# Performance work log

Hardware: AMD Instinct MI355X
Metric: run time of the kernel (lower is better)

The kernel has to match this reference:

```python
import jax, jax.numpy as jnp
import numpy as np

KNOTS = 8
INTERVAL = 4.0
LAYERS = 8
WIDTH = 128
DX = 64
DY = 64
P = 3 * KNOTS - 1  # widths(K) + heights(K) + interior derivatives(K-1)
BATCH = 16384
MIN_DERIV = 1e-3
SOFTMAX_ADJ = 1e-2


def _made_masks(D, W):
    in_deg = np.arange(1, D + 1)
    hid_deg = (np.arange(W) % max(D - 1, 1)) + 1
    m1 = (hid_deg[:, None] >= in_deg[None, :]).astype(np.float32)        # (W, D)
    out_deg = np.repeat(np.arange(1, D + 1), P)                           # (D*P,)
    m2 = (out_deg[:, None] > hid_deg[None, :]).astype(np.float32)        # (D*P, W)
    return jnp.asarray(m1), jnp.asarray(m2)


def _adj_softmax(v):
    p = jax.nn.softmax(v, axis=-1)
    return (p + SOFTMAX_ADJ / v.shape[-1]) / (1.0 + SOFTMAX_ADJ)


def _rqs_transform(x, params):
    # x: (B, D); params: (B, D, P). Rational-quadratic spline on [-B_int, B_int], identity outside.
    Bi = INTERVAL
    w = params[..., :KNOTS]
    h = params[..., KNOTS:2 * KNOTS]
    d = params[..., 2 * KNOTS:]
    widths = _adj_softmax(w) * 2 * Bi
    heights = _adj_softmax(h) * 2 * Bi
    zero = jnp.zeros(x.shape + (1,), x.dtype)
    x_pos = -Bi + jnp.concatenate([zero, jnp.cumsum(widths, -1)], -1)   # (B, D, K+1)
    y_pos = -Bi + jnp.concatenate([zero, jnp.cumsum(heights, -1)], -1)
    derivs = jax.nn.softplus(d) + MIN_DERIV                              # (B, D, K-1)
    one = jnp.ones(x.shape + (1,), x.dtype)
    derivs = jnp.concatenate([one, derivs, one], -1)                     # (B, D, K+1), boundary derivs = 1
    inside = (x > -Bi) & (x < Bi)
    xc = jnp.clip(x, -Bi, Bi)
    # bin search (K is small; vectorized comparison)
    k = jnp.clip(jnp.sum((xc[..., None] >= x_pos), -1) - 1, 0, KNOTS - 1)

    def g(a, i):
        return jnp.take_along_axis(a, i[..., None], -1)[..., 0]

    xk, xk1 = g(x_pos, k), g(x_pos, k + 1)
    yk, yk1 = g(y_pos, k), g(y_pos, k + 1)
    dk, dk1 = g(derivs, k), g(derivs, k + 1)
    sk = (yk1 - yk) / (xk1 - xk)
    xi = (xc - xk) / (xk1 - xk)
    omx = 1.0 - xi
    den = sk + (dk1 + dk - 2.0 * sk) * xi * omx
    out = yk + (yk1 - yk) * (sk * xi * xi + dk * xi * omx) / den
    ld = 2.0 * jnp.log(sk) + jnp.log(dk1 * xi * xi + 2.0 * sk * xi * omx + dk * omx * omx) - 2.0 * jnp.log(den)
    return jnp.where(inside, out, x), jnp.where(inside, ld, 0.0)


def _maf_transform(x, W1, b1, Wout, bout, D):
    # Stacked layers: masked MLP -> elementwise RQ spline -> reverse permutation.
    m1, m2 = _made_masks(D, WIDTH)

    def layer(carry, ws):
        xc, ld = carry
        w1, bb1, wo, bo = ws
        hdn = jax.nn.relu(xc @ (w1 * m1).T + bb1)                # (B, W)
        p = (hdn @ (wo * m2).T + bo).reshape(xc.shape[0], D, P)  # (B, D, P)
        x2, ldj = _rqs_transform(xc, p)
        return (x2[:, ::-1], ld + ldj.sum(-1)), None

    init = (x, jnp.zeros(x.shape[0], x.dtype))
    (xf, ld), _ = jax.lax.scan(layer, init, (W1, b1, Wout, bout))
    return xf, ld


def setup_inputs() -> dict:
    key = jax.random.key(0)
    ks = jax.random.split(key, 10)
    s = 0.05
    return {
        "x": jax.random.normal(ks[0], (BATCH, DX), jnp.float32),
        "y": jax.random.normal(ks[1], (BATCH, DY), jnp.float32),
        "f_W1": jax.random.normal(ks[2], (LAYERS, WIDTH, DX), jnp.float32) * s,
        "f_b1": jnp.zeros((LAYERS, WIDTH), jnp.float32),
        "f_Wout": jax.random.normal(ks[3], (LAYERS, DX * P, WIDTH), jnp.float32) * s,
        "f_bout": jnp.zeros((LAYERS, DX * P), jnp.float32),
        "g_W1": jax.random.normal(ks[4], (LAYERS, WIDTH, DY), jnp.float32) * s,
        "g_b1": jnp.zeros((LAYERS, WIDTH), jnp.float32),
        "g_Wout": jax.random.normal(ks[5], (LAYERS, DY * P, WIDTH), jnp.float32) * s,
        "g_bout": jnp.zeros((LAYERS, DY * P), jnp.float32),
    }


def reference(x, y, f_W1, f_b1, f_Wout, f_bout, g_W1, g_b1, g_Wout, g_bout):
    xo, ldf = _maf_transform(x, f_W1, f_b1, f_Wout, f_bout, DX)
    yo, ldg = _maf_transform(y, g_W1, g_b1, g_Wout, g_bout, DY)
    return (xo, ldf, yo, ldg)
```

## Files before the change

kernel.cpp:

```cpp
#include <hip/hip_runtime.h>
#include <math.h>

#define BATCH   16384
#define DIMS    64
#define WID     128
#define KN      8
#define NP      23
#define NCOL    (DIMS * NP)
#define NLAYERS 8
#define BI_F    4.0f
#define GRP     92
#define NGRP    16
#define XPITCH  68
#define LOG2E   1.44269504f

#define PF_WOUT (NLAYERS * NCOL * WID)
#define PF_W1   (NLAYERS * WID * DIMS)

typedef short s16x8 __attribute__((ext_vector_type(8)));
typedef float f32x4 __attribute__((ext_vector_type(4)));

__device__ __forceinline__ unsigned short f2bf(float f) {
    unsigned int u = __builtin_bit_cast(unsigned int, f);
    unsigned int r = (u + 0x7FFFu + ((u >> 16) & 1u)) >> 16;
    return (unsigned short)r;
}
__device__ __forceinline__ float bf2f(unsigned short u) {
    return __builtin_bit_cast(float, (unsigned int)u << 16);
}
__device__ __forceinline__ unsigned int cvtpk_bf16(float a, float b) {
    unsigned int r;
    asm("v_cvt_pk_bf16_f32 %0, %1, %2" : "=v"(r) : "v"(a), "v"(b));
    return r;
}

__device__ __forceinline__ void stage16(const unsigned short* g, unsigned short* l) {
    __builtin_amdgcn_global_load_lds(
        (__attribute__((address_space(1))) void*)g,
        (__attribute__((address_space(3))) void*)l,
        16, 0, 0);
}

__global__ __launch_bounds__(256) void premask_kernel(
    const float* __restrict__ f_wout, const float* __restrict__ g_wout,
    const float* __restrict__ f_w1,   const float* __restrict__ g_w1,
    unsigned short* __restrict__ womask, unsigned short* __restrict__ w1mask)
{
    const int idx    = blockIdx.x * 256 + threadIdx.x;
    const int stride = gridDim.x * 256;

    const int totw = 2 * PF_WOUT;
    for (int i = idx; i < totw; i += stride) {
        int fl = i / PF_WOUT;
        int r  = i % PF_WOUT;
        int h  = r % WID;
        int o  = (r / WID) % NCOL;
        int d  = o / NP;
        int hd = h % (DIMS - 1) + 1;
        const float* src = fl ? g_wout : f_wout;
        unsigned short v = (hd <= d) ? f2bf(src[r] * LOG2E) : (unsigned short)0;
        const int dst = i - h + (h ^ ((o & 7) << 4));
        womask[dst] = v;
    }

    const int tot1 = 2 * PF_W1;
    for (int i = idx; i < tot1; i += stride) {
        int fl = i / PF_W1;
        int r  = i % PF_W1;
        int c  = r % DIMS;
        int w  = (r / DIMS) % WID;
        int deg = w % (DIMS - 1) + 1;
        const float* src = fl ? g_w1 : f_w1;
        w1mask[i] = (c < deg) ? f2bf(src[r]) : (unsigned short)0;
    }
}

__global__ __launch_bounds__(256)
__attribute__((amdgpu_waves_per_eu(2, 2)))
void flow8_kernel(
    const float* __restrict__ xin_f, const float* __restrict__ xin_g,
    float* __restrict__ xout_f,      float* __restrict__ xout_g,
    const unsigned short* __restrict__ w1m_f, const unsigned short* __restrict__ w1m_g,
    const float* __restrict__ b1_f,  const float* __restrict__ b1_g,
    const unsigned short* __restrict__ wom_f, const unsigned short* __restrict__ wom_g,
    const float* __restrict__ bo_f,  const float* __restrict__ bo_g,
    float* __restrict__ ld_f,        float* __restrict__ ld_g)
{
    __shared__ __align__(16) unsigned short Wl[GRP * WID];
    __shared__ __align__(16) unsigned short S[4][2176];
    __shared__ __align__(16) float Xf[2][4][16][XPITCH];

    const int t    = threadIdx.x;
    const int wv   = t >> 6;
    const int ln   = t & 63;
    const int m    = ln & 15;
    const int q    = ln >> 4;
    const int flow = blockIdx.y;
    const int r0   = blockIdx.x * 64 + wv * 16;

    const float* xin          = flow ? xin_g : xin_f;
    float*       xout         = flow ? xout_g : xout_f;
    const unsigned short* w1m = flow ? w1m_g : w1m_f;
    const float* b1           = flow ? b1_g  : b1_f;
    const unsigned short* wom = flow ? wom_g : wom_f;
    const float* bo           = flow ? bo_g  : bo_f;
    float*       ldp          = flow ? ld_g  : ld_f;

    {
        const int row = ln >> 2;
        const int c0  = (ln & 3) * 16;
        const float* srcr = xin + (size_t)(r0 + row) * DIMS + c0;
        float* dstr = &Xf[0][wv][row][c0];
        #pragma unroll
        for (int i = 0; i < 4; ++i)
            *(float4*)(dstr + i * 4) = *(const float4*)(srcr + i * 4);
    }
    asm volatile("" ::: "memory");

    {
        const unsigned short* src = wom + ln * 8;
        #pragma unroll
        for (int i = 0; i < 6; ++i) {
            const int c = wv + 4 * i;
            if (c < 23) stage16(src + c * 512, Wl + c * 512);
        }
    }

    float bnx[6];
    #pragma unroll
    for (int nt = 0; nt < 6; ++nt)
        bnx[nt] = bo[nt * 16 + m] * LOG2E;

    float ldsum = 0.0f;
    int cur = 0;
    unsigned short* sw = &S[wv][0];

    __syncthreads();

    #pragma unroll 1
    for (int l = 0; l < NLAYERS; ++l) {
        const unsigned short* w1m_l = w1m + (size_t)l * WID * DIMS;
        const float* b1_l           = b1 + (size_t)l * WID;
        const int nxt = cur ^ 1;

        s16x8 xa[2];
        #pragma unroll
        for (int ks = 0; ks < 2; ++ks) {
            float4 v0 = *(const float4*)&Xf[cur][wv][m][ks * 32 + q * 8];
            float4 v1 = *(const float4*)&Xf[cur][wv][m][ks * 32 + q * 8 + 4];
            uint4 uu;
            uu.x = cvtpk_bf16(v0.x, v0.y);
            uu.y = cvtpk_bf16(v0.z, v0.w);
            uu.z = cvtpk_bf16(v1.x, v1.y);
            uu.w = cvtpk_bf16(v1.z, v1.w);
            xa[ks] = __builtin_bit_cast(s16x8, uu);
        }

        f32x4 hacc[8];
        #pragma unroll
        for (int nt = 0; nt < 8; ++nt) {
            float bv = b1_l[nt * 16 + m];
            hacc[nt] = (f32x4){bv, bv, bv, bv};
        }
        #pragma unroll
        for (int ks = 0; ks < 2; ++ks) {
            #pragma unroll
            for (int nt = 0; nt < 8; ++nt) {
                s16x8 bfr = *(const s16x8*)(w1m_l + (nt * 16 + m) * DIMS + ks * 32 + q * 8);
                hacc[nt] = __builtin_amdgcn_mfma_f32_16x16x32_bf16(xa[ks], bfr, hacc[nt], 0, 0, 0);
            }
        }
        #pragma unroll
        for (int nt = 0; nt < 8; ++nt) {
            const int c = nt * 16 + m;
            unsigned int p0 = cvtpk_bf16(fmaxf(hacc[nt][0], 0.0f),
                                         fmaxf(hacc[nt][1], 0.0f));
            unsigned int p1 = cvtpk_bf16(fmaxf(hacc[nt][2], 0.0f),
                                         fmaxf(hacc[nt][3], 0.0f));
            sw[(q * 4 + 0) * 136 + c] = (unsigned short)p0;
            sw[(q * 4 + 1) * 136 + c] = (unsigned short)(p0 >> 16);
            sw[(q * 4 + 2) * 136 + c] = (unsigned short)p1;
            sw[(q * 4 + 3) * 136 + c] = (unsigned short)(p1 >> 16);
        }
        asm volatile("" ::: "memory");

        s16x8 af[4];
        #pragma unroll
        for (int ks = 0; ks < 4; ++ks)
            af[ks] = *(const s16x8*)&sw[m * 136 + ks * 32 + q * 8];
        asm volatile("" ::: "memory");

        #pragma unroll 1
        for (int g = 0; g < NGRP; ++g) {
            const int gi = l * NGRP + g;

            f32x4 acc[6];
            #pragma unroll
            for (int nt = 0; nt < 6; ++nt)
                acc[nt] = (f32x4){bnx[nt], bnx[nt], bnx[nt], bnx[nt]};

            const int swz = ((g * 4 + m) & 7) << 4;
            #pragma unroll
            for (int ks = 0; ks < 4; ++ks) {
                #pragma unroll
                for (int nt = 0; nt < 6; ++nt) {
                    const s16x8 bfr = *(const s16x8*)&Wl[
                        (nt * 16 + m) * WID + ((ks * 32 + q * 8) ^ swz)];
                    acc[nt] = __builtin_amdgcn_mfma_f32_16x16x32_bf16(af[ks], bfr, acc[nt], 0, 0, 0);
                }
            }

            if (gi < NLAYERS * NGRP - 1) {
                __syncthreads();
                const int l2 = (gi + 1) >> 4;
                const int g2 = (gi + 1) & 15;
                const unsigned short* src = wom +
                    ((size_t)l2 * NCOL + (size_t)g2 * GRP) * WID + ln * 8;
                #pragma unroll
                for (int i = 0; i < 6; ++i) {
                    const int c = wv + 4 * i;
                    if (c < 23) stage16(src + c * 512, Wl + c * 512);
                }
                #pragma unroll
                for (int nt = 0; nt < 6; ++nt) {
                    int o = g2 * GRP + nt * 16 + m;
                    o = (o < NCOL) ? o : (NCOL - 1);
                    bnx[nt] = bo[(size_t)l2 * NCOL + o] * LOG2E;
                }
            }

            #pragma unroll
            for (int nt = 0; nt < 6; ++nt) {
                const int c18 = (nt * 16 + m) * 18 + q * 4;
                unsigned int p0 = cvtpk_bf16(acc[nt][0], acc[nt][1]);
                unsigned int p1 = cvtpk_bf16(acc[nt][2], acc[nt][3]);
                sw[c18 + 0] = (unsigned short)p0;
                sw[c18 + 1] = (unsigned short)(p0 >> 16);
                sw[c18 + 2] = (unsigned short)p1;
                sw[c18 + 3] = (unsigned short)(p1 >> 16);
            }

            {
                const int d = g * 4 + q;

                float pp[NP];
                #pragma unroll
                for (int j = 0; j < NP; ++j)
                    pp[j] = bf2f(sw[(q * 23 + j) * 18 + m]);

                const float xraw = Xf[cur][wv][m][d];

                float ew[KN], eh[KN];
                #pragma unroll
                for (int j = 0; j < KN; ++j) {
                    ew[j] = exp2f(pp[j]);
                    eh[j] = exp2f(pp[8 + j]);
                }
                const float sw_ = ((ew[0] + ew[1]) + (ew[2] + ew[3]))
                                + ((ew[4] + ew[5]) + (ew[6] + ew[7]));
                const float sh_ = ((eh[0] + eh[1]) + (eh[2] + eh[3]))
                                + ((eh[4] + eh[5]) + (eh[6] + eh[7]));
                const float cmul = 8.0f / 1.01f;
                const float cadd = 0.00125f * (8.0f / 1.01f);
                const float rw = cmul / sw_, rh = cmul / sh_;
                float width[KN], height[KN];
                #pragma unroll
                for (int j = 0; j < KN; ++j) {
                    width[j]  = fmaf(ew[j], rw, cadd);
                    height[j] = fmaf(eh[j], rh, cadd);
                }
                float dv[KN + 1];
                dv[0] = 1.0f; dv[KN] = 1.0f;
                #pragma unroll
                for (int i = 1; i < KN; ++i) {
                    const float tt = exp2f(pp[15 + i]);
                    dv[i] = fmaf(__log2f(1.0f + tt), 0.69314718f, 0.001f);
                }

                const bool inside = (xraw > -BI_F) && (xraw < BI_F);
                const float xcl = fminf(fmaxf(xraw, -BI_F), BI_F);

                float cx = -BI_F + width[0], cy = -BI_F + height[0];
                float xk = -BI_F, yk = -BI_F, xk1 = cx, yk1 = cy;
                float dk = 1.0f, dk1 = dv[1];
                #pragma unroll
                for (int i = 1; i < KN; ++i) {
                    const float nx = cx + width[i];
                    const float ny = cy + height[i];
                    const bool cc = (xcl >= cx);
                    xk  = cc ? cx : xk;    yk  = cc ? cy : yk;
                    xk1 = cc ? nx : xk1;   yk1 = cc ? ny : yk1;
                    dk  = cc ? dv[i] : dk; dk1 = cc ? dv[i + 1] : dk1;
                    cx = nx; cy = ny;
                }

                const float invw = 1.0f / (xk1 - xk);
                const float sk   = (yk1 - yk) * invw;
                const float xi   = (xcl - xk) * invw;
                const float omx  = 1.0f - xi;
                const float den  = sk + (dk1 + dk - 2.0f * sk) * xi * omx;
                const float rden = 1.0f / den;
                float outv = fmaf((yk1 - yk) * (sk * xi * xi + dk * xi * omx), rden, yk);
                const float numl = dk1 * xi * xi + 2.0f * sk * xi * omx + dk * omx * omx;
                float ldj = __logf(sk * sk * numl * rden * rden);
                outv = inside ? outv : xraw;
                ldj  = inside ? ldj : 0.0f;

                Xf[nxt][wv][m][DIMS - 1 - d] = outv;
                ldsum += ldj;
            }

            if (gi < NLAYERS * NGRP - 1) {
                __syncthreads();
            }
        }

        cur ^= 1;
    }

    asm volatile("" ::: "memory");

    {
        const int row = ln >> 2;
        const int c0  = (ln & 3) * 16;
        const float* srcr = &Xf[cur][wv][row][c0];
        float* dstr = xout + (size_t)(r0 + row) * DIMS + c0;
        #pragma unroll
        for (int i = 0; i < 4; ++i)
            *(float4*)(dstr + i * 4) = *(const float4*)(srcr + i * 4);
    }

    float v = ldsum + __shfl_xor(ldsum, 16, 64);
    v = v + __shfl_xor(v, 32, 64);
    if (ln < 16) {
        ldp[r0 + ln] = v;
    }
}

extern "C" void kernel_launch(void* const* d_in, const int* in_sizes, int n_in,
                              void* d_out, int out_size, void* d_ws, size_t ws_size,
                              hipStream_t stream)
{
    const float* x      = (const float*)d_in[0];
    const float* y      = (const float*)d_in[1];
    const float* f_W1   = (const float*)d_in[2];
    const float* f_b1   = (const float*)d_in[3];
    const float* f_Wout = (const float*)d_in[4];
    const float* f_bout = (const float*)d_in[5];
    const float* g_W1   = (const float*)d_in[6];
    const float* g_b1   = (const float*)d_in[7];
    const float* g_Wout = (const float*)d_in[8];
    const float* g_bout = (const float*)d_in[9];

    float* out = (float*)d_out;
    float* xo  = out;
    float* ldf = out + (size_t)BATCH * DIMS;
    float* yo  = ldf + BATCH;
    float* ldg = yo + (size_t)BATCH * DIMS;

    unsigned short* womask = (unsigned short*)d_ws;
    unsigned short* w1mask = womask + 2 * (size_t)PF_WOUT;

    premask_kernel<<<dim3(2048), dim3(256), 0, stream>>>(
        f_Wout, g_Wout, f_W1, g_W1, womask, w1mask);

    flow8_kernel<<<dim3(BATCH / 64, 2), dim3(256), 0, stream>>>(
        x, y, xo, yo,
        w1mask, w1mask + (size_t)PF_W1,
        f_b1, g_b1,
        womask, womask + (size_t)PF_WOUT,
        f_bout, g_bout,
        ldf, ldg);
}
```

Measured before the change: 438.3 us.

## Transpose spline param scratch for vector LDS reads and compute softplus lazily

Changes the per-wave LDS scratch layout so each lane's 23 spline parameters sit contiguously, with a padded pitch and an offset per 23-column group. Each lane then fetches them with three 16-byte vector loads instead of 23 scalar ushort loads. It also evaluates softplus only for the two selected bin derivatives rather than all seven interior ones, cutting transcendental work. The cost is scattered scalar stores on the write side and possible LDS bank conflicts from the new pitch.

```diff
diff --git a/kernel.cpp b/kernel.cpp
--- a/kernel.cpp
+++ b/kernel.cpp
@@ -12,12 +12,14 @@
 #define GRP     92
 #define NGRP    16
 #define XPITCH  68
+#define PCP     104
 #define LOG2E   1.44269504f
 
 #define PF_WOUT (NLAYERS * NCOL * WID)
 #define PF_W1   (NLAYERS * WID * DIMS)
 
 typedef short s16x8 __attribute__((ext_vector_type(8)));
+typedef unsigned short u16x8 __attribute__((ext_vector_type(8)));
 typedef float f32x4 __attribute__((ext_vector_type(4)));
 
 __device__ __forceinline__ unsigned short f2bf(float f) {
@@ -25,8 +27,11 @@
     unsigned int r = (u + 0x7FFFu + ((u >> 16) & 1u)) >> 16;
     return (unsigned short)r;
 }
-__device__ __forceinline__ float bf2f(unsigned short u) {
-    return __builtin_bit_cast(float, (unsigned int)u << 16);
+__device__ __forceinline__ float bfLO(unsigned int u) {
+    return __builtin_bit_cast(float, u << 16);
+}
+__device__ __forceinline__ float bfHI(unsigned int u) {
+    return __builtin_bit_cast(float, u & 0xffff0000u);
 }
 __device__ __forceinline__ unsigned int cvtpk_bf16(float a, float b) {
     unsigned int r;
@@ -131,6 +136,13 @@
     for (int nt = 0; nt < 6; ++nt)
         bnx[nt] = bo[nt * 16 + m] * LOG2E;
 
+    int offn[6];
+    #pragma unroll
+    for (int nt = 0; nt < 6; ++nt) {
+        const int o = nt * 16 + m;
+        offn[nt] = o + (o >= 23) + (o >= 46) + (o >= 69) + (o >= 92);
+    }
+
     float ldsum = 0.0f;
     int cur = 0;
     unsigned short* sw = &S[wv][0];
@@ -231,22 +243,40 @@
 
             #pragma unroll
             for (int nt = 0; nt < 6; ++nt) {
-                const int c18 = (nt * 16 + m) * 18 + q * 4;
+                const int cb = q * 4 * PCP + offn[nt];
                 unsigned int p0 = cvtpk_bf16(acc[nt][0], acc[nt][1]);
                 unsigned int p1 = cvtpk_bf16(acc[nt][2], acc[nt][3]);
-                sw[c18 + 0] = (unsigned short)p0;
-                sw[c18 + 1] = (unsigned short)(p0 >> 16);
-                sw[c18 + 2] = (unsigned short)p1;
-                sw[c18 + 3] = (unsigned short)(p1 >> 16);
-            }
+                sw[cb          ] = (unsigned short)p0;
+                sw[cb +     PCP] = (unsigned short)(p0 >> 16);
+                sw[cb + 2 * PCP] = (unsigned short)p1;
+                sw[cb + 3 * PCP] = (unsigned short)(p1 >> 16);
+            }
+            asm volatile("" ::: "memory");
 
             {
                 const int d = g * 4 + q;
 
+                const unsigned short* pr = &sw[m * PCP + q * 24];
+                u16x8 w0 = *(const u16x8*)(pr);
+                u16x8 w1 = *(const u16x8*)(pr + 8);
+                u16x8 w2 = *(const u16x8*)(pr + 16);
+                uint4 r0 = __builtin_bit_cast(uint4, w0);
+                uint4 r1 = __builtin_bit_cast(uint4, w1);
+                uint4 r2 = __builtin_bit_cast(uint4, w2);
+
                 float pp[NP];
-                #pragma unroll
-                for (int j = 0; j < NP; ++j)
-                    pp[j] = bf2f(sw[(q * 23 + j) * 18 + m]);
+                pp[0]  = bfLO(r0.x); pp[1]  = bfHI(r0.x);
+                pp[2]  = bfLO(r0.y); pp[3]  = bfHI(r0.y);
+                pp[4]  = bfLO(r0.z); pp[5]  = bfHI(r0.z);
+                pp[6]  = bfLO(r0.w); pp[7]  = bfHI(r0.w);
+                pp[8]  = bfLO(r1.x); pp[9]  = bfHI(r1.x);
+                pp[10] = bfLO(r1.y); pp[11] = bfHI(r1.y);
+                pp[12] = bfLO(r1.z); pp[13] = bfHI(r1.z);
+                pp[14] = bfLO(r1.w); pp[15] = bfHI(r1.w);
+                pp[16] = bfLO(r2.x); pp[17] = bfHI(r2.x);
+                pp[18] = bfLO(r2.y); pp[19] = bfHI(r2.y);
+                pp[20] = bfLO(r2.z); pp[21] = bfHI(r2.z);
+                pp[22] = bfLO(r2.w);
 
                 const float xraw = Xf[cur][wv][m][d];
 
@@ -269,30 +299,33 @@
                     width[j]  = fmaf(ew[j], rw, cadd);
                     height[j] = fmaf(eh[j], rh, cadd);
                 }
-                float dv[KN + 1];
-                dv[0] = 1.0f; dv[KN] = 1.0f;
-                #pragma unroll
-                for (int i = 1; i < KN; ++i) {
-                    const float tt = exp2f(pp[15 + i]);
-                    dv[i] = fmaf(__log2f(1.0f + tt), 0.69314718f, 0.001f);
-                }
 
                 const bool inside = (xraw > -BI_F) && (xraw < BI_F);
                 const float xcl = fminf(fmaxf(xraw, -BI_F), BI_F);
 
                 float cx = -BI_F + width[0], cy = -BI_F + height[0];
                 float xk = -BI_F, yk = -BI_F, xk1 = cx, yk1 = cy;
-                float dk = 1.0f, dk1 = dv[1];
+                float selk = pp[16], selk1 = pp[16];
+                bool cc1 = false, cc7 = false;
                 #pragma unroll
                 for (int i = 1; i < KN; ++i) {
                     const float nx = cx + width[i];
                     const float ny = cy + height[i];
                     const bool cc = (xcl >= cx);
+                    if (i == 1) cc1 = cc;
+                    if (i == 7) cc7 = cc;
                     xk  = cc ? cx : xk;    yk  = cc ? cy : yk;
                     xk1 = cc ? nx : xk1;   yk1 = cc ? ny : yk1;
-                    dk  = cc ? dv[i] : dk; dk1 = cc ? dv[i + 1] : dk1;
+                    selk = cc ? pp[15 + i] : selk;
+                    if (i < 7) selk1 = cc ? pp[16 + i] : selk1;
                     cx = nx; cy = ny;
                 }
+                const float ta = exp2f(selk);
+                const float da = fmaf(__log2f(1.0f + ta), 0.69314718f, 0.001f);
+                const float tb = exp2f(selk1);
+                const float db = fmaf(__log2f(1.0f + tb), 0.69314718f, 0.001f);
+                const float dk  = cc1 ? da : 1.0f;
+                const float dk1 = cc7 ? 1.0f : db;
 
                 const float invw = 1.0f / (xk1 - xk);
                 const float sk   = (yk1 - yk) * invw;
```

Result: faster. 427.2 us (-2.5%).
